# Kernel tuning notes

Hardware: AMD Instinct MI355X
Metric: run time of the kernel (lower is better)

## Reference

```python
import jax, jax.numpy as jnp
import numpy as np

N_NODES = 100000
N_CLIQUES = 50000
N_EDGES = 1600000
D_IN = 128
D_OUT = 128


def setup_inputs() -> dict:
    key = jax.random.key(0)
    k1, k2, k3, k4, k5, k6 = jax.random.split(key, 6)
    x = jax.random.normal(k1, (N_NODES, D_IN), dtype=jnp.float32)
    x_clique = jax.random.normal(k2, (N_CLIQUES, D_IN), dtype=jnp.float32)
    node_idx = jax.random.randint(k3, (N_EDGES,), 0, N_NODES, dtype=jnp.int64)
    clique_idx = jax.random.randint(k4, (N_EDGES,), 0, N_CLIQUES, dtype=jnp.int64)
    node2clique_index = jnp.stack([node_idx, clique_idx], axis=0)
    # Linear(in, out): weight [out, in], bias [out]
    W = jax.random.normal(k5, (D_OUT, D_IN), dtype=jnp.float32) * (1.0 / np.sqrt(D_IN))
    b = jax.random.normal(k6, (D_OUT,), dtype=jnp.float32) * 0.01
    return {"x": x, "x_clique": x_clique, "node2clique_index": node2clique_index, "W": W, "b": b}


def reference(x, x_clique, node2clique_index, W, b):
    node_idx = node2clique_index[0]
    clique_idx = node2clique_index[1]
    n_nodes = x.shape[0]
    gathered = x_clique[clique_idx]                                   # [E, D_in]
    summed = jax.ops.segment_sum(gathered, node_idx, num_segments=n_nodes)  # [N, D_in]
    count = jax.ops.segment_sum(
        jnp.ones((gathered.shape[0],), dtype=x_clique.dtype), node_idx, num_segments=n_nodes
    )
    mean = summed / jnp.maximum(count, 1.0)[:, None]                  # scatter-mean, count clamped like torch_scatter
    out = mean @ W.T + b                                              # Linear
    return out
```

## Files before the change

kernel.cpp:

```cpp
#include <hip/hip_runtime.h>


typedef short bf16x8 __attribute__((ext_vector_type(8)));
typedef float f32x4  __attribute__((ext_vector_type(4)));
typedef float f32x2  __attribute__((ext_vector_type(2)));
typedef unsigned long long u64;

#define BK_SHIFT 8
#define NB_MAX 512
#define RAWCAP 4608
#define PADCAP 6400
#define FCHUNK 4096

__device__ inline ushort f2b(float f) {
    union { float f; uint u; } v; v.f = f;
    uint r = v.u + 0x7FFFu + ((v.u >> 16) & 1u);
    return (ushort)(r >> 16);
}
__device__ inline float blo(uint v) { union { uint u; float f; } x; x.u = v << 16;        return x.f; }
__device__ inline float bhi(uint v) { union { uint u; float f; } x; x.u = v & 0xFFFF0000u; return x.f; }

struct FillSM {
    int cnt[NB_MAX];
    int sloc[NB_MAX];
    int gbase[NB_MAX];
    int cur[NB_MAX];
    int wtot[8];
    u64 stage[FCHUNK];
};
struct TransSM { ushort wl[128 * 128]; };

__global__ __launch_bounds__(512) void k_front(const float* __restrict__ xc,
                                               const float* __restrict__ W,
                                               ushort* __restrict__ yb, int nc,
                                               const int* __restrict__ nidx,
                                               const int* __restrict__ cidx,
                                               int* __restrict__ bcur,
                                               u64* __restrict__ pairs,
                                               int ne, int gf) {
    __shared__ union USM { FillSM f; TransSM tr; } sm;
    const int t = threadIdx.x;

    if ((int)blockIdx.x < gf) {
        const int e0 = blockIdx.x * FCHUNK;
        const int e1 = min(e0 + FCHUNK, ne);
        sm.f.cnt[t] = 0;
        sm.f.cur[t] = 0;
        __syncthreads();

        int nn[8], cc[8];
        #pragma unroll
        for (int k = 0; k < 8; ++k) {
            int i = e0 + k * 512 + t;
            if (i < e1) {
                nn[k] = nidx[i];
                cc[k] = cidx[i];
                atomicAdd(&sm.f.cnt[nn[k] >> BK_SHIFT], 1);
            } else nn[k] = -1;
        }
        __syncthreads();

        const int lane = t & 63, wid = t >> 6;
        int v = sm.f.cnt[t];
        int inc = v;
        #pragma unroll
        for (int d = 1; d < 64; d <<= 1) {
            int x = __shfl_up(inc, d);
            if (lane >= d) inc += x;
        }
        if (lane == 63) sm.f.wtot[wid] = inc;
        __syncthreads();
        int wpre = 0;
        for (int i = 0; i < wid; ++i) wpre += sm.f.wtot[i];
        int excl = wpre + inc - v;
        sm.f.sloc[t] = excl;
        if (v > 0) sm.f.gbase[t] = t * RAWCAP + atomicAdd(&bcur[t], v);
        __syncthreads();

        #pragma unroll
        for (int k = 0; k < 8; ++k) {
            if (nn[k] >= 0) {
                int b = nn[k] >> BK_SHIFT;
                int slot = sm.f.sloc[b] + atomicAdd(&sm.f.cur[b], 1);
                sm.f.stage[slot] = (u64)(uint)nn[k] | ((u64)(uint)cc[k] << 32);
            }
        }
        __syncthreads();

        const int m = e1 - e0;
        for (int i = t; i < m; i += 512) {
            u64 p = sm.f.stage[i];
            int b = (int)((uint)p >> BK_SHIFT);
            pairs[(size_t)sm.f.gbase[b] + (i - sm.f.sloc[b])] = p;
        }
    } else {
        const int bid = blockIdx.x - gf;
        for (int i = 0; i < 8; ++i) {
            int idx = (i * 512 + t) * 4;
            float4 w4 = *reinterpret_cast<const float4*>(&W[idx]);
            int o = idx >> 7, k = idx & 127;
            ushort4 h;
            h.x = f2b(w4.x); h.y = f2b(w4.y); h.z = f2b(w4.z); h.w = f2b(w4.w);
            int byte = o * 256 + k * 2;
            byte ^= (o & 7) << 4;
            *reinterpret_cast<ushort4*>(reinterpret_cast<char*>(sm.tr.wl) + byte) = h;
        }
        __syncthreads();

        const int wid = t >> 6, lane = t & 63;
        const int lrow = lane & 15;
        const int lk = lane >> 4;
        const int r0 = bid * 128 + wid * 16;
        const bool rowok = (r0 + lrow) < nc;
        const float* arow = &xc[(size_t)(r0 + lrow) * 128];

        bf16x8 afrag[4];
        for (int kb = 0; kb < 4; ++kb) {
            float4 a0 = make_float4(0.f, 0.f, 0.f, 0.f), a1 = a0;
            if (rowok) {
                int k0 = kb * 32 + lk * 8;
                a0 = *reinterpret_cast<const float4*>(&arow[k0]);
                a1 = *reinterpret_cast<const float4*>(&arow[k0 + 4]);
            }
            bf16x8 a;
            a[0] = (short)f2b(a0.x); a[1] = (short)f2b(a0.y);
            a[2] = (short)f2b(a0.z); a[3] = (short)f2b(a0.w);
            a[4] = (short)f2b(a1.x); a[5] = (short)f2b(a1.y);
            a[6] = (short)f2b(a1.z); a[7] = (short)f2b(a1.w);
            afrag[kb] = a;
        }

        for (int ct = 0; ct < 8; ++ct) {
            f32x4 c = {0.f, 0.f, 0.f, 0.f};
            const int o = ct * 16 + lrow;
            #pragma unroll
            for (int kb = 0; kb < 4; ++kb) {
                int byte = o * 256 + (kb * 32 + lk * 8) * 2;
                byte ^= (o & 7) << 4;
                bf16x8 bb = *reinterpret_cast<const bf16x8*>(reinterpret_cast<const char*>(sm.tr.wl) + byte);
                c = __builtin_amdgcn_mfma_f32_16x16x32_bf16(afrag[kb], bb, c, 0, 0, 0);
            }
            const int orow = r0 + lk * 4;
            #pragma unroll
            for (int j = 0; j < 4; ++j)
                if (orow + j < nc)
                    yb[(size_t)(orow + j) * 128 + ct * 16 + lrow] = f2b(c[j]);
        }
    }
}

__global__ __launch_bounds__(256) void k_build(const u64* __restrict__ pairs,
                                               const int* __restrict__ bcur,
                                               int* __restrict__ offsets,
                                               int* __restrict__ ncnt,
                                               int* __restrict__ edge_dst,
                                               ushort* __restrict__ yb,
                                               int n_nodes, int nc) {
    __shared__ int arr[256], nexcl[256], cur[256], wtot[4];
    __shared__ int mpad_sh;
    __shared__ int scidx[PADCAP];
    const int b = blockIdx.x, t = threadIdx.x;
    const int p0r = b * RAWCAP;
    const int p0e = b * PADCAP;
    const int m = min(bcur[b], RAWCAP);
    const int node0 = b << BK_SHIFT;

    if (b == 0 && t < 32)
        reinterpret_cast<uint2*>(&yb[(size_t)nc * 128])[t] = make_uint2(0u, 0u);

    arr[t] = 0; cur[t] = 0;
    __syncthreads();
    for (int i = t; i < m; i += 256)
        atomicAdd(&arr[(int)((uint)pairs[p0r + i]) & 255], 1);
    __syncthreads();

    const int lane = t & 63, wid = t >> 6;
    const int v = arr[t];
    const int pv = (v + 7) & ~7;
    int inc = pv;
    #pragma unroll
    for (int d = 1; d < 64; d <<= 1) {
        int x = __shfl_up(inc, d);
        if (lane >= d) inc += x;
    }
    if (lane == 63) wtot[wid] = inc;
    __syncthreads();
    int wpre = 0;
    for (int i = 0; i < wid; ++i) wpre += wtot[i];
    const int excl = wpre + inc - pv;
    nexcl[t] = excl;
    if (node0 + t < n_nodes) {
        offsets[node0 + t] = p0e + excl;
        ncnt[node0 + t] = v;
    }
    if (t == 255) mpad_sh = excl + pv;
    __syncthreads();

    for (int i = t; i < m; i += 256) {
        u64 p = pairs[p0r + i];
        int l = (int)((uint)p) & 255;
        int slot = nexcl[l] + atomicAdd(&cur[l], 1);
        scidx[slot] = (int)(p >> 32);
    }
    __syncthreads();
    for (int k = v; k < pv; ++k)
        scidx[excl + k] = nc;
    __syncthreads();
    const int mp = mpad_sh;
    for (int i = t; i < mp; i += 256)
        edge_dst[p0e + i] = scidx[i];
}

__global__ __launch_bounds__(256) void k_reduce(const ushort* __restrict__ yb,
                                                const int* __restrict__ offsets,
                                                const int* __restrict__ ncnt,
                                                const int* __restrict__ edge_dst,
                                                const float* __restrict__ bias,
                                                float* __restrict__ out, int n) {
    int gw = (blockIdx.x * blockDim.x + threadIdx.x) >> 6;
    if (gw >= n) return;
    const int lane = threadIdx.x & 63;
    const int gwu = __builtin_amdgcn_readfirstlane(gw);
    const int s = offsets[gwu];
    const int cnt = ncnt[gwu];
    const int e = s + ((cnt + 7) & ~7);
    const char* ybase = reinterpret_cast<const char*>(yb) + lane * 4;

    float ax0 = 0.f, ay0 = 0.f, ax1 = 0.f, ay1 = 0.f;
    int j = s;
    for (; j + 16 <= e; j += 16) {
        uint v[16];
        #pragma unroll
        for (int u = 0; u < 16; ++u) {
            int c = edge_dst[j + u];
            v[u] = *reinterpret_cast<const uint*>(ybase + (size_t)c * 256);
        }
        #pragma unroll
        for (int u = 0; u < 16; u += 2) {
            ax0 += blo(v[u]);     ay0 += bhi(v[u]);
            ax1 += blo(v[u + 1]); ay1 += bhi(v[u + 1]);
        }
    }
    if (j < e) {
        uint v[8];
        #pragma unroll
        for (int u = 0; u < 8; ++u) {
            int c = edge_dst[j + u];
            v[u] = *reinterpret_cast<const uint*>(ybase + (size_t)c * 256);
        }
        #pragma unroll
        for (int u = 0; u < 8; u += 2) {
            ax0 += blo(v[u]);     ay0 += bhi(v[u]);
            ax1 += blo(v[u + 1]); ay1 += bhi(v[u + 1]);
        }
    }
    float ax = ax0 + ax1, ay = ay0 + ay1;
    float inv = 1.0f / (float)max(cnt, 1);
    f32x2 bv = *reinterpret_cast<const f32x2*>(&bias[lane * 2]);
    f32x2 o;
    o.x = ax * inv + bv.x;
    o.y = ay * inv + bv.y;
    __builtin_nontemporal_store(o, reinterpret_cast<f32x2*>(&out[(size_t)gw * 128 + lane * 2]));
}

extern "C" void kernel_launch(void* const* d_in, const int* in_sizes, int n_in,
                              void* d_out, int out_size, void* d_ws, size_t ws_size,
                              hipStream_t stream) {
    const float* xc  = (const float*)d_in[1];
    const int*   n2c = (const int*)d_in[2];
    const float* W   = (const float*)d_in[3];
    const float* b   = (const float*)d_in[4];
    float* out = (float*)d_out;

    const int n_nodes   = in_sizes[0] / 128;
    const int n_cliques = in_sizes[1] / 128;
    const int n_edges   = in_sizes[2] / 2;
    const int* nidx = n2c;
    const int* cidx = n2c + n_edges;
    const int nbucket = (n_nodes + ((1 << BK_SHIFT) - 1)) >> BK_SHIFT;

    char* ws = (char*)d_ws;
    size_t off = 0;
    ushort* yb = (ushort*)(ws + off);   off += (size_t)(n_cliques + 1) * 128 * sizeof(ushort);
    off = (off + 15) & ~(size_t)15;
    u64* pairs = (u64*)(ws + off);      off += (size_t)nbucket * RAWCAP * sizeof(u64);
    int* edge_dst = (int*)(ws + off);   off += (size_t)nbucket * PADCAP * sizeof(int);
    int* offsets = (int*)(ws + off);    off += (size_t)n_nodes * sizeof(int);
    int* ncnt = (int*)(ws + off);       off += (size_t)n_nodes * sizeof(int);
    int* bcur = (int*)(ws + off);       off += (size_t)NB_MAX * sizeof(int);

    (void)hipMemsetAsync(bcur, 0, (size_t)NB_MAX * sizeof(int), stream);

    const int gf = (n_edges + FCHUNK - 1) / FCHUNK;
    const int gt = (n_cliques + 127) / 128;
    k_front<<<gf + gt, 512, 0, stream>>>(xc, W, yb, n_cliques, nidx, cidx, bcur, pairs, n_edges, gf);
    k_build<<<nbucket, 256, 0, stream>>>(pairs, bcur, offsets, ncnt, edge_dst, yb, n_nodes, n_cliques);
    k_reduce<<<(n_nodes * 64 + 255) / 256, 256, 0, stream>>>(yb, offsets, ncnt, edge_dst, b, out, n_nodes);
}
```

Measured before the change: 94.71 us.

## Fuse CSR build and gather-reduce into one kernel with packed 32-bit pairs

Merges the bucket-build and reduce kernels into a single kernel that sorts each bucket's edges in LDS and immediately gathers and averages from shared memory. This removes the global edge_dst/offsets/ncnt round trip and one launch. Pairs shrink from 64-bit to 32-bit, packing local node (7 bits) and clique index (17 bits), and bucket size halves to 128 nodes, giving 1024 buckets. In exchange each block has only 8 waves, each handling 16 nodes serially, which can limit parallelism and latency hiding in the gather. The packing also assumes clique indices fit in 17 bits.

```diff
diff --git a/kernel.cpp b/kernel.cpp
--- a/kernel.cpp
+++ b/kernel.cpp
@@ -4,12 +4,11 @@
 typedef short bf16x8 __attribute__((ext_vector_type(8)));
 typedef float f32x4  __attribute__((ext_vector_type(4)));
 typedef float f32x2  __attribute__((ext_vector_type(2)));
-typedef unsigned long long u64;
-
-#define BK_SHIFT 8
-#define NB_MAX 512
-#define RAWCAP 4608
-#define PADCAP 6400
+
+#define BK_SHIFT 7
+#define NBMAX 1024
+#define CAPR 2432
+#define PADLDS 3328
 #define FCHUNK 4096
 
 __device__ inline ushort f2b(float f) {
@@ -21,12 +20,13 @@
 __device__ inline float bhi(uint v) { union { uint u; float f; } x; x.u = v & 0xFFFF0000u; return x.f; }
 
 struct FillSM {
-    int cnt[NB_MAX];
-    int sloc[NB_MAX];
-    int gbase[NB_MAX];
-    int cur[NB_MAX];
-    int wtot[8];
-    u64 stage[FCHUNK];
+    int cnt[NBMAX];
+    int sloc[NBMAX];
+    int gbase[NBMAX];
+    int cur[NBMAX];
+    int wtot[16];
+    uint   stage[FCHUNK];
+    ushort sbkt[FCHUNK];
 };
 struct TransSM { ushort wl[128 * 128]; };
 
@@ -36,16 +36,17 @@
                                                const int* __restrict__ nidx,
                                                const int* __restrict__ cidx,
                                                int* __restrict__ bcur,
-                                               u64* __restrict__ pairs,
-                                               int ne, int gf) {
+                                               uint* __restrict__ pairs,
+                                               int ne, int gf, int nbucket) {
     __shared__ union USM { FillSM f; TransSM tr; } sm;
     const int t = threadIdx.x;
+    const int lane = t & 63, wid = t >> 6;
 
     if ((int)blockIdx.x < gf) {
         const int e0 = blockIdx.x * FCHUNK;
         const int e1 = min(e0 + FCHUNK, ne);
-        sm.f.cnt[t] = 0;
-        sm.f.cur[t] = 0;
+        sm.f.cnt[t] = 0;       sm.f.cnt[t + 512] = 0;
+        sm.f.cur[t] = 0;       sm.f.cur[t + 512] = 0;
         __syncthreads();
 
         int nn[8], cc[8];
@@ -60,21 +61,26 @@
         }
         __syncthreads();
 
-        const int lane = t & 63, wid = t >> 6;
-        int v = sm.f.cnt[t];
-        int inc = v;
-        #pragma unroll
-        for (int d = 1; d < 64; d <<= 1) {
-            int x = __shfl_up(inc, d);
-            if (lane >= d) inc += x;
-        }
-        if (lane == 63) sm.f.wtot[wid] = inc;
-        __syncthreads();
-        int wpre = 0;
-        for (int i = 0; i < wid; ++i) wpre += sm.f.wtot[i];
-        int excl = wpre + inc - v;
-        sm.f.sloc[t] = excl;
-        if (v > 0) sm.f.gbase[t] = t * RAWCAP + atomicAdd(&bcur[t], v);
+        const int v0 = sm.f.cnt[t];
+        const int v1 = sm.f.cnt[t + 512];
+        int inc0 = v0;
+        #pragma unroll
+        for (int d = 1; d < 64; d <<= 1) { int x = __shfl_up(inc0, d); if (lane >= d) inc0 += x; }
+        if (lane == 63) sm.f.wtot[wid] = inc0;
+        int inc1 = v1;
+        #pragma unroll
+        for (int d = 1; d < 64; d <<= 1) { int x = __shfl_up(inc1, d); if (lane >= d) inc1 += x; }
+        if (lane == 63) sm.f.wtot[8 + wid] = inc1;
+        __syncthreads();
+        int S1 = 0;
+        for (int i = 0; i < 8; ++i) S1 += sm.f.wtot[i];
+        int wpre0 = 0, wpre1 = S1;
+        for (int i = 0; i < wid; ++i) { wpre0 += sm.f.wtot[i]; wpre1 += sm.f.wtot[8 + i]; }
+        sm.f.sloc[t] = wpre0 + inc0 - v0;
+        sm.f.sloc[t + 512] = wpre1 + inc1 - v1;
+        if (v0 > 0) sm.f.gbase[t] = t * CAPR + atomicAdd(&bcur[t], v0);
+        if (t + 512 < nbucket && v1 > 0)
+            sm.f.gbase[t + 512] = (t + 512) * CAPR + atomicAdd(&bcur[t + 512], v1);
         __syncthreads();
 
         #pragma unroll
@@ -82,19 +88,21 @@
             if (nn[k] >= 0) {
                 int b = nn[k] >> BK_SHIFT;
                 int slot = sm.f.sloc[b] + atomicAdd(&sm.f.cur[b], 1);
-                sm.f.stage[slot] = (u64)(uint)nn[k] | ((u64)(uint)cc[k] << 32);
+                sm.f.stage[slot] = ((uint)(nn[k] & 127) << 17) | (uint)cc[k];
+                sm.f.sbkt[slot] = (ushort)b;
             }
         }
         __syncthreads();
 
         const int m = e1 - e0;
         for (int i = t; i < m; i += 512) {
-            u64 p = sm.f.stage[i];
-            int b = (int)((uint)p >> BK_SHIFT);
-            pairs[(size_t)sm.f.gbase[b] + (i - sm.f.sloc[b])] = p;
+            int b = sm.f.sbkt[i];
+            pairs[(size_t)sm.f.gbase[b] + (i - sm.f.sloc[b])] = sm.f.stage[i];
         }
     } else {
         const int bid = blockIdx.x - gf;
+        if (bid == 0 && t < 64)
+            reinterpret_cast<uint*>(&yb[(size_t)nc * 128])[t] = 0u;
         for (int i = 0; i < 8; ++i) {
             int idx = (i * 512 + t) * 4;
             float4 w4 = *reinterpret_cast<const float4*>(&W[idx]);
@@ -107,7 +115,6 @@
         }
         __syncthreads();
 
-        const int wid = t >> 6, lane = t & 63;
         const int lrow = lane & 15;
         const int lk = lane >> 4;
         const int r0 = bid * 128 + wid * 16;
@@ -149,118 +156,101 @@
     }
 }
 
-__global__ __launch_bounds__(256) void k_build(const u64* __restrict__ pairs,
+__global__ __launch_bounds__(512) void k_fused(const uint* __restrict__ pairs,
                                                const int* __restrict__ bcur,
-                                               int* __restrict__ offsets,
-                                               int* __restrict__ ncnt,
-                                               int* __restrict__ edge_dst,
-                                               ushort* __restrict__ yb,
+                                               const ushort* __restrict__ yb,
+                                               const float* __restrict__ bias,
+                                               float* __restrict__ out,
                                                int n_nodes, int nc) {
-    __shared__ int arr[256], nexcl[256], cur[256], wtot[4];
-    __shared__ int mpad_sh;
-    __shared__ int scidx[PADCAP];
+    __shared__ int arr[128], pexcl[128], cur[128];
+    __shared__ int wtot2[2];
+    __shared__ int scidx[PADLDS];
     const int b = blockIdx.x, t = threadIdx.x;
-    const int p0r = b * RAWCAP;
-    const int p0e = b * PADCAP;
-    const int m = min(bcur[b], RAWCAP);
+    const int lane = t & 63, wid = t >> 6;
+    const int g0 = b * CAPR;
+    const int m = min(bcur[b], CAPR);
     const int node0 = b << BK_SHIFT;
 
-    if (b == 0 && t < 32)
-        reinterpret_cast<uint2*>(&yb[(size_t)nc * 128])[t] = make_uint2(0u, 0u);
-
-    arr[t] = 0; cur[t] = 0;
-    __syncthreads();
-    for (int i = t; i < m; i += 256)
-        atomicAdd(&arr[(int)((uint)pairs[p0r + i]) & 255], 1);
-    __syncthreads();
-
-    const int lane = t & 63, wid = t >> 6;
-    const int v = arr[t];
-    const int pv = (v + 7) & ~7;
-    int inc = pv;
-    #pragma unroll
-    for (int d = 1; d < 64; d <<= 1) {
-        int x = __shfl_up(inc, d);
-        if (lane >= d) inc += x;
-    }
-    if (lane == 63) wtot[wid] = inc;
-    __syncthreads();
-    int wpre = 0;
-    for (int i = 0; i < wid; ++i) wpre += wtot[i];
-    const int excl = wpre + inc - pv;
-    nexcl[t] = excl;
-    if (node0 + t < n_nodes) {
-        offsets[node0 + t] = p0e + excl;
-        ncnt[node0 + t] = v;
-    }
-    if (t == 255) mpad_sh = excl + pv;
-    __syncthreads();
-
-    for (int i = t; i < m; i += 256) {
-        u64 p = pairs[p0r + i];
-        int l = (int)((uint)p) & 255;
-        int slot = nexcl[l] + atomicAdd(&cur[l], 1);
-        scidx[slot] = (int)(p >> 32);
-    }
-    __syncthreads();
-    for (int k = v; k < pv; ++k)
-        scidx[excl + k] = nc;
-    __syncthreads();
-    const int mp = mpad_sh;
-    for (int i = t; i < mp; i += 256)
-        edge_dst[p0e + i] = scidx[i];
-}
-
-__global__ __launch_bounds__(256) void k_reduce(const ushort* __restrict__ yb,
-                                                const int* __restrict__ offsets,
-                                                const int* __restrict__ ncnt,
-                                                const int* __restrict__ edge_dst,
-                                                const float* __restrict__ bias,
-                                                float* __restrict__ out, int n) {
-    int gw = (blockIdx.x * blockDim.x + threadIdx.x) >> 6;
-    if (gw >= n) return;
-    const int lane = threadIdx.x & 63;
-    const int gwu = __builtin_amdgcn_readfirstlane(gw);
-    const int s = offsets[gwu];
-    const int cnt = ncnt[gwu];
-    const int e = s + ((cnt + 7) & ~7);
+    if (t < 128) { arr[t] = 0; cur[t] = 0; }
+    __syncthreads();
+    for (int i = t; i < m; i += 512)
+        atomicAdd(&arr[pairs[g0 + i] >> 17], 1);
+    __syncthreads();
+
+    int v = 0, pv = 0, inc = 0;
+    if (t < 128) {
+        v = arr[t];
+        pv = (v + 7) & ~7;
+        inc = pv;
+        #pragma unroll
+        for (int d = 1; d < 64; d <<= 1) { int x = __shfl_up(inc, d); if (lane >= d) inc += x; }
+        if (lane == 63) wtot2[wid] = inc;
+    }
+    __syncthreads();
+    if (t < 128) {
+        int wpre = (wid == 1) ? wtot2[0] : 0;
+        pexcl[t] = wpre + inc - pv;
+    }
+    __syncthreads();
+
+    for (int i = t; i < m; i += 512) {
+        uint p = pairs[g0 + i];
+        int l = (int)(p >> 17);
+        int slot = pexcl[l] + atomicAdd(&cur[l], 1);
+        scidx[slot] = (int)(p & 0x1FFFFu);
+    }
+    __syncthreads();
+    if (t < 128) {
+        int base = pexcl[t];
+        for (int k = v; k < pv; ++k) scidx[base + k] = nc;
+    }
+    __syncthreads();
+
     const char* ybase = reinterpret_cast<const char*>(yb) + lane * 4;
-
-    float ax0 = 0.f, ay0 = 0.f, ax1 = 0.f, ay1 = 0.f;
-    int j = s;
-    for (; j + 16 <= e; j += 16) {
-        uint v[16];
-        #pragma unroll
-        for (int u = 0; u < 16; ++u) {
-            int c = edge_dst[j + u];
-            v[u] = *reinterpret_cast<const uint*>(ybase + (size_t)c * 256);
-        }
-        #pragma unroll
-        for (int u = 0; u < 16; u += 2) {
-            ax0 += blo(v[u]);     ay0 += bhi(v[u]);
-            ax1 += blo(v[u + 1]); ay1 += bhi(v[u + 1]);
-        }
-    }
-    if (j < e) {
-        uint v[8];
-        #pragma unroll
-        for (int u = 0; u < 8; ++u) {
-            int c = edge_dst[j + u];
-            v[u] = *reinterpret_cast<const uint*>(ybase + (size_t)c * 256);
-        }
-        #pragma unroll
-        for (int u = 0; u < 8; u += 2) {
-            ax0 += blo(v[u]);     ay0 += bhi(v[u]);
-            ax1 += blo(v[u + 1]); ay1 += bhi(v[u + 1]);
-        }
-    }
-    float ax = ax0 + ax1, ay = ay0 + ay1;
-    float inv = 1.0f / (float)max(cnt, 1);
-    f32x2 bv = *reinterpret_cast<const f32x2*>(&bias[lane * 2]);
-    f32x2 o;
-    o.x = ax * inv + bv.x;
-    o.y = ay * inv + bv.y;
-    __builtin_nontemporal_store(o, reinterpret_cast<f32x2*>(&out[(size_t)gw * 128 + lane * 2]));
+    for (int li = wid * 16; li < wid * 16 + 16; ++li) {
+        const int node = node0 + li;
+        const int cnt = arr[li];
+        const int e = (cnt + 7) & ~7;
+        const int base = pexcl[li];
+
+        float ax0 = 0.f, ay0 = 0.f, ax1 = 0.f, ay1 = 0.f;
+        int j = 0;
+        for (; j + 16 <= e; j += 16) {
+            uint vv[16];
+            #pragma unroll
+            for (int u = 0; u < 16; ++u) {
+                int c = scidx[base + j + u];
+                vv[u] = *reinterpret_cast<const uint*>(ybase + (size_t)c * 256);
+            }
+            #pragma unroll
+            for (int u = 0; u < 16; u += 2) {
+                ax0 += blo(vv[u]);     ay0 += bhi(vv[u]);
+                ax1 += blo(vv[u + 1]); ay1 += bhi(vv[u + 1]);
+            }
+        }
+        if (j < e) {
+            uint vv[8];
+            #pragma unroll
+            for (int u = 0; u < 8; ++u) {
+                int c = scidx[base + j + u];
+                vv[u] = *reinterpret_cast<const uint*>(ybase + (size_t)c * 256);
+            }
+            #pragma unroll
+            for (int u = 0; u < 8; u += 2) {
+                ax0 += blo(vv[u]);     ay0 += bhi(vv[u]);
+                ax1 += blo(vv[u + 1]); ay1 += bhi(vv[u + 1]);
+            }
+        }
+        if (node < n_nodes) {
+            float ax = ax0 + ax1, ay = ay0 + ay1;
+            float inv = 1.0f / (float)max(cnt, 1);
+            f32x2 bv = *reinterpret_cast<const f32x2*>(&bias[lane * 2]);
+            f32x2 o;
+            o.x = ax * inv + bv.x;
+            o.y = ay * inv + bv.y;
+            __builtin_nontemporal_store(o, reinterpret_cast<f32x2*>(&out[(size_t)node * 128 + lane * 2]));
+        }
+    }
 }
 
 extern "C" void kernel_launch(void* const* d_in, const int* in_sizes, int n_in,
@@ -283,17 +273,14 @@
     size_t off = 0;
     ushort* yb = (ushort*)(ws + off);   off += (size_t)(n_cliques + 1) * 128 * sizeof(ushort);
     off = (off + 15) & ~(size_t)15;
-    u64* pairs = (u64*)(ws + off);      off += (size_t)nbucket * RAWCAP * sizeof(u64);
-    int* edge_dst = (int*)(ws + off);   off += (size_t)nbucket * PADCAP * sizeof(int);
-    int* offsets = (int*)(ws + off);    off += (size_t)n_nodes * sizeof(int);
-    int* ncnt = (int*)(ws + off);       off += (size_t)n_nodes * sizeof(int);
-    int* bcur = (int*)(ws + off);       off += (size_t)NB_MAX * sizeof(int);
-
-    (void)hipMemsetAsync(bcur, 0, (size_t)NB_MAX * sizeof(int), stream);
+    uint* pairs = (uint*)(ws + off);    off += (size_t)nbucket * CAPR * sizeof(uint);
+    int* bcur = (int*)(ws + off);       off += (size_t)NBMAX * sizeof(int);
+
+    (void)hipMemsetAsync(bcur, 0, (size_t)NBMAX * sizeof(int), stream);
 
     const int gf = (n_edges + FCHUNK - 1) / FCHUNK;
     const int gt = (n_cliques + 127) / 128;
-    k_front<<<gf + gt, 512, 0, stream>>>(xc, W, yb, n_cliques, nidx, cidx, bcur, pairs, n_edges, gf);
-    k_build<<<nbucket, 256, 0, stream>>>(pairs, bcur, offsets, ncnt, edge_dst, yb, n_nodes, n_cliques);
-    k_reduce<<<(n_nodes * 64 + 255) / 256, 256, 0, stream>>>(yb, offsets, ncnt, edge_dst, b, out, n_nodes);
-}
+    k_front<<<gf + gt, 512, 0, stream>>>(xc, W, yb, n_cliques, nidx, cidx, bcur,
+                                         pairs, n_edges, gf, nbucket);
+    k_fused<<<nbucket, 512, 0, stream>>>(pairs, bcur, yb, b, out, n_nodes, n_cliques);
+}
```

Result: slower. 107.5 us (+13.5%).

## Pack edge pairs into 32-bit words and pad bucket counters apart

Applied to the files above, without the earlier changes.

Edge pairs staged between the fill and build kernels are packed into one 32-bit word (8-bit local node id plus 24-bit clique id) instead of a 64-bit pair. This halves the global scatter and read traffic for the pair buffer, and the shared-memory staging now keeps the bucket index in a separate array. Global bucket counters are strided 16 ints apart so the atomics no longer contend on the same cache lines. Zeroing of the padding row moves from the build kernel to the transform blocks. The packing assumes fewer than 2^24 cliques.

```diff
diff --git a/kernel.cpp b/kernel.cpp
--- a/kernel.cpp
+++ b/kernel.cpp
@@ -4,10 +4,10 @@
 typedef short bf16x8 __attribute__((ext_vector_type(8)));
 typedef float f32x4  __attribute__((ext_vector_type(4)));
 typedef float f32x2  __attribute__((ext_vector_type(2)));
-typedef unsigned long long u64;
 
 #define BK_SHIFT 8
 #define NB_MAX 512
+#define BCUR_STRIDE 16
 #define RAWCAP 4608
 #define PADCAP 6400
 #define FCHUNK 4096
@@ -26,7 +26,8 @@
     int gbase[NB_MAX];
     int cur[NB_MAX];
     int wtot[8];
-    u64 stage[FCHUNK];
+    uint   stage[FCHUNK];
+    ushort sbkt[FCHUNK];
 };
 struct TransSM { ushort wl[128 * 128]; };
 
@@ -36,10 +37,11 @@
                                                const int* __restrict__ nidx,
                                                const int* __restrict__ cidx,
                                                int* __restrict__ bcur,
-                                               u64* __restrict__ pairs,
+                                               uint* __restrict__ pairs,
                                                int ne, int gf) {
     __shared__ union USM { FillSM f; TransSM tr; } sm;
     const int t = threadIdx.x;
+    const int lane = t & 63, wid = t >> 6;
 
     if ((int)blockIdx.x < gf) {
         const int e0 = blockIdx.x * FCHUNK;
@@ -60,21 +62,17 @@
         }
         __syncthreads();
 
-        const int lane = t & 63, wid = t >> 6;
         int v = sm.f.cnt[t];
         int inc = v;
         #pragma unroll
-        for (int d = 1; d < 64; d <<= 1) {
-            int x = __shfl_up(inc, d);
-            if (lane >= d) inc += x;
-        }
+        for (int d = 1; d < 64; d <<= 1) { int x = __shfl_up(inc, d); if (lane >= d) inc += x; }
         if (lane == 63) sm.f.wtot[wid] = inc;
         __syncthreads();
         int wpre = 0;
         for (int i = 0; i < wid; ++i) wpre += sm.f.wtot[i];
         int excl = wpre + inc - v;
         sm.f.sloc[t] = excl;
-        if (v > 0) sm.f.gbase[t] = t * RAWCAP + atomicAdd(&bcur[t], v);
+        if (v > 0) sm.f.gbase[t] = t * RAWCAP + atomicAdd(&bcur[t * BCUR_STRIDE], v);
         __syncthreads();
 
         #pragma unroll
@@ -82,19 +80,21 @@
             if (nn[k] >= 0) {
                 int b = nn[k] >> BK_SHIFT;
                 int slot = sm.f.sloc[b] + atomicAdd(&sm.f.cur[b], 1);
-                sm.f.stage[slot] = (u64)(uint)nn[k] | ((u64)(uint)cc[k] << 32);
+                sm.f.stage[slot] = ((uint)(nn[k] & 255) << 24) | (uint)cc[k];
+                sm.f.sbkt[slot] = (ushort)b;
             }
         }
         __syncthreads();
 
         const int m = e1 - e0;
         for (int i = t; i < m; i += 512) {
-            u64 p = sm.f.stage[i];
-            int b = (int)((uint)p >> BK_SHIFT);
-            pairs[(size_t)sm.f.gbase[b] + (i - sm.f.sloc[b])] = p;
+            int b = sm.f.sbkt[i];
+            pairs[(size_t)sm.f.gbase[b] + (i - sm.f.sloc[b])] = sm.f.stage[i];
         }
     } else {
         const int bid = blockIdx.x - gf;
+        if (bid == 0 && t < 64)
+            reinterpret_cast<uint*>(&yb[(size_t)nc * 128])[t] = 0u;
         for (int i = 0; i < 8; ++i) {
             int idx = (i * 512 + t) * 4;
             float4 w4 = *reinterpret_cast<const float4*>(&W[idx]);
@@ -107,7 +107,6 @@
         }
         __syncthreads();
 
-        const int wid = t >> 6, lane = t & 63;
         const int lrow = lane & 15;
         const int lk = lane >> 4;
         const int r0 = bid * 128 + wid * 16;
@@ -149,12 +148,11 @@
     }
 }
 
-__global__ __launch_bounds__(256) void k_build(const u64* __restrict__ pairs,
+__global__ __launch_bounds__(256) void k_build(const uint* __restrict__ pairs,
                                                const int* __restrict__ bcur,
                                                int* __restrict__ offsets,
                                                int* __restrict__ ncnt,
                                                int* __restrict__ edge_dst,
-                                               ushort* __restrict__ yb,
                                                int n_nodes, int nc) {
     __shared__ int arr[256], nexcl[256], cur[256], wtot[4];
     __shared__ int mpad_sh;
@@ -162,16 +160,13 @@
     const int b = blockIdx.x, t = threadIdx.x;
     const int p0r = b * RAWCAP;
     const int p0e = b * PADCAP;
-    const int m = min(bcur[b], RAWCAP);
+    const int m = min(bcur[b * BCUR_STRIDE], RAWCAP);
     const int node0 = b << BK_SHIFT;
 
-    if (b == 0 && t < 32)
-        reinterpret_cast<uint2*>(&yb[(size_t)nc * 128])[t] = make_uint2(0u, 0u);
-
     arr[t] = 0; cur[t] = 0;
     __syncthreads();
     for (int i = t; i < m; i += 256)
-        atomicAdd(&arr[(int)((uint)pairs[p0r + i]) & 255], 1);
+        atomicAdd(&arr[pairs[p0r + i] >> 24], 1);
     __syncthreads();
 
     const int lane = t & 63, wid = t >> 6;
@@ -197,10 +192,10 @@
     __syncthreads();
 
     for (int i = t; i < m; i += 256) {
-        u64 p = pairs[p0r + i];
-        int l = (int)((uint)p) & 255;
+        uint p = pairs[p0r + i];
+        int l = (int)(p >> 24);
         int slot = nexcl[l] + atomicAdd(&cur[l], 1);
-        scidx[slot] = (int)(p >> 32);
+        scidx[slot] = (int)(p & 0xFFFFFFu);
     }
     __syncthreads();
     for (int k = v; k < pv; ++k)
@@ -283,17 +278,19 @@
     size_t off = 0;
     ushort* yb = (ushort*)(ws + off);   off += (size_t)(n_cliques + 1) * 128 * sizeof(ushort);
     off = (off + 15) & ~(size_t)15;
-    u64* pairs = (u64*)(ws + off);      off += (size_t)nbucket * RAWCAP * sizeof(u64);
+    uint* pairs = (uint*)(ws + off);    off += (size_t)nbucket * RAWCAP * sizeof(uint);
     int* edge_dst = (int*)(ws + off);   off += (size_t)nbucket * PADCAP * sizeof(int);
     int* offsets = (int*)(ws + off);    off += (size_t)n_nodes * sizeof(int);
     int* ncnt = (int*)(ws + off);       off += (size_t)n_nodes * sizeof(int);
-    int* bcur = (int*)(ws + off);       off += (size_t)NB_MAX * sizeof(int);
-
-    (void)hipMemsetAsync(bcur, 0, (size_t)NB_MAX * sizeof(int), stream);
+    int* bcur = (int*)(ws + off);       off += (size_t)NB_MAX * BCUR_STRIDE * sizeof(int);
+
+    (void)hipMemsetAsync(bcur, 0, (size_t)NB_MAX * BCUR_STRIDE * sizeof(int), stream);
 
     const int gf = (n_edges + FCHUNK - 1) / FCHUNK;
     const int gt = (n_cliques + 127) / 128;
-    k_front<<<gf + gt, 512, 0, stream>>>(xc, W, yb, n_cliques, nidx, cidx, bcur, pairs, n_edges, gf);
-    k_build<<<nbucket, 256, 0, stream>>>(pairs, bcur, offsets, ncnt, edge_dst, yb, n_nodes, n_cliques);
+    k_front<<<gf + gt, 512, 0, stream>>>(xc, W, yb, n_cliques, nidx, cidx, bcur,
+                                         pairs, n_edges, gf);
+    k_build<<<nbucket, 256, 0, stream>>>(pairs, bcur, offsets, ncnt, edge_dst,
+                                         n_nodes, n_cliques);
     k_reduce<<<(n_nodes * 64 + 255) / 256, 256, 0, stream>>>(yb, offsets, ncnt, edge_dst, b, out, n_nodes);
 }
```

Measured after the change: 99.61 us. 1.05x slower.
